# Performance work log

Hardware: AMD Instinct MI355X
Metric: run time of the kernel (lower is better)

The kernel has to match this reference:

```python
import jax, jax.numpy as jnp
import numpy as np

NUM_ROUTES = 1152
NUM_CAPS = 10
CAPS_IN = 8
CAPS_DIM = 16
BATCH = 128
NUM_IT = 3


def _squash(s):
    # s: [..., caps_dim]; scale = |s|^2 / ((1+|s|^2) * |s|)
    sqn = jnp.sum(s * s, axis=-1, keepdims=True)
    return s * (sqn / ((1.0 + sqn) * jnp.sqrt(sqn)))


def setup_inputs() -> dict:
    key = jax.random.key(0)
    k1, k2 = jax.random.split(key)
    x = jax.random.normal(k1, (BATCH, NUM_ROUTES, CAPS_IN), dtype=jnp.float32)
    W = jax.random.normal(k2, (1, NUM_ROUTES, NUM_CAPS, CAPS_DIM, CAPS_IN), dtype=jnp.float32)
    return {"input": x, "W": W}


def reference(input, W):
    # u_hat[b,r,j,d] = W[r,j,d,c] @ x[b,r,c]  (original broadcasts W over batch)
    u_hat = jnp.einsum('rjdc,brc->brjd', W[0], input)
    r, j = u_hat.shape[1], u_hat.shape[2]
    b_ij = jnp.zeros((r, j), dtype=u_hat.dtype)  # shared across batch, as in original
    v = None
    for _ in range(NUM_IT):
        c_ij = jax.nn.softmax(b_ij, axis=1)          # softmax over num_caps (dim=2 orig)
        s = jnp.einsum('rj,brjd->bjd', c_ij, u_hat)  # weighted sum over routes
        v = _squash(s)                                # [bs, num_caps, caps_dim]
        # agreement: <u_hat, v> averaged over batch (original updates every iter)
        b_ij = b_ij + jnp.mean(jnp.einsum('brjd,bjd->brj', u_hat, v), axis=0)
    return v[..., None]  # [bs, num_caps, caps_dim, 1], matches v_j.squeeze(1) shape
```

## Files before the change

### kernel.cpp

```cpp
#include <hip/hip_runtime.h>
#include <math.h>

#define R_ROUTES 1152
#define N_CAPS 10
#define C_IN 8
#define D_DIM 16
#define B_BATCH 128
#define JD 160
#define KK 9216
#define KSPLIT 48
#define RS 24
#define NG 5
#define BH 2

typedef __attribute__((ext_vector_type(8))) short short8;
typedef __attribute__((ext_vector_type(4))) float f32x4;

__device__ inline unsigned short f2bf(float f) {
    unsigned int u = __float_as_uint(f);
    unsigned int r = u + 0x7FFFu + ((u >> 16) & 1u);
    return (unsigned short)(r >> 16);
}
__device__ inline float bf2f(unsigned short h) {
    return __uint_as_float(((unsigned int)h) << 16);
}


__global__ __launch_bounds__(256) void k_prep0(
    const float* __restrict__ x, const float* __restrict__ W,
    unsigned short* __restrict__ xT, f32x4* __restrict__ zbase) {
    __shared__ float tile[32][33];
    int id = blockIdx.x, t = threadIdx.x;
    if (id < 288) {
        int bx = id;
        int tx = t & 31, ty = t >> 5;
        for (int by = 0; by < 4; by++) {
            if (by) __syncthreads();
#pragma unroll
            for (int i = 0; i < 4; i++) {
                int row = ty + i * 8;
                tile[row][tx] = x[(size_t)(by * 32 + row) * KK + bx * 32 + tx];
            }
            __syncthreads();
#pragma unroll
            for (int i = 0; i < 4; i++) {
                int row = ty + i * 8;
                xT[(size_t)(bx * 32 + row) * B_BATCH + by * 32 + tx] = f2bf(tile[tx][row]);
            }
        }
        return;
    }
    if (id < 348) {
        int idx = (id - 288) * 256 + t;
        zbase[idx] = (f32x4){0.f, 0.f, 0.f, 0.f};
        return;
    }
    int wb = id - 348;
    const f32x4* wp = (const f32x4*)W;
    size_t base = (size_t)wb * 3840 + t;
#pragma unroll
    for (int i = 0; i < 15; i++) {
        f32x4 v = wp[base + i * 256];
        asm volatile("" :: "v"(v[0]), "v"(v[1]), "v"(v[2]), "v"(v[3]));
    }
}

template <int FIRST>
__global__ __launch_bounds__(256) void k_iter(
    const float* __restrict__ x, const float* __restrict__ W,
    const float* __restrict__ ctab, float* __restrict__ s) {
    int t = threadIdx.x;
    int ks = blockIdx.x, ng = blockIdx.y, bh = blockIdx.z;
    int r0 = ks * RS, jd0 = ng * 32, b_base = bh * 64;
    int w = t >> 6, l = t & 63, row = l & 15, quad = l >> 4;
    const float* px = x + (size_t)(b_base + w * 16 + row) * KK + ks * 192;
    f32x4 acc0 = {0,0,0,0}, acc1 = {0,0,0,0};
#pragma unroll
    for (int st = 0; st < 6; st++) {
        int rr = r0 + st * 4 + quad;
        float c0 = FIRST ? 0.1f : ctab[rr * N_CAPS + (jd0 >> 4)];
        float c1 = FIRST ? 0.1f : ctab[rr * N_CAPS + (jd0 >> 4) + 1];
        const float4* wp0 = (const float4*)(W + ((size_t)rr * JD + jd0 + row) * C_IN);
        const float4* wp1 = (const float4*)(W + ((size_t)rr * JD + jd0 + 16 + row) * C_IN);
        float4 wa = wp0[0], wb = wp0[1], wc = wp1[0], wd = wp1[1];
        float wv0[8] = {wa.x,wa.y,wa.z,wa.w, wb.x,wb.y,wb.z,wb.w};
        float wv1[8] = {wc.x,wc.y,wc.z,wc.w, wd.x,wd.y,wd.z,wd.w};
        short8 Bh0, Bh1;
#pragma unroll
        for (int i = 0; i < 8; i++) {
            Bh0[i] = (short)f2bf(wv0[i] * c0);
            Bh1[i] = (short)f2bf(wv1[i] * c1);
        }
        float4 x0 = *(const float4*)(px + st * 32 + quad * 8);
        float4 x1 = *(const float4*)(px + st * 32 + quad * 8 + 4);
        float xv[8] = {x0.x,x0.y,x0.z,x0.w, x1.x,x1.y,x1.z,x1.w};
        short8 Ah, Al;
#pragma unroll
        for (int i = 0; i < 8; i++) {
            unsigned short h = f2bf(xv[i]);
            Ah[i] = (short)h;
            Al[i] = (short)f2bf(xv[i] - bf2f(h));
        }
        acc0 = __builtin_amdgcn_mfma_f32_16x16x32_bf16(Ah, Bh0, acc0, 0, 0, 0);
        acc0 = __builtin_amdgcn_mfma_f32_16x16x32_bf16(Al, Bh0, acc0, 0, 0, 0);
        acc1 = __builtin_amdgcn_mfma_f32_16x16x32_bf16(Ah, Bh1, acc1, 0, 0, 0);
        acc1 = __builtin_amdgcn_mfma_f32_16x16x32_bf16(Al, Bh1, acc1, 0, 0, 0);
    }
#pragma unroll
    for (int i = 0; i < 4; i++) {
        int b0 = b_base + w * 16 + quad * 4 + i;
        atomicAdd(&s[(size_t)b0 * JD + jd0 + row],      acc0[i]);
        atomicAdd(&s[(size_t)b0 * JD + jd0 + 16 + row], acc1[i]);
    }
}

template <int ACCUM>
__global__ __launch_bounds__(256) void k_va(
    const unsigned short* __restrict__ xT, const float* __restrict__ s_prev,
    const float* __restrict__ W, float* __restrict__ b_ij,
    float* __restrict__ ctab) {
    __shared__ unsigned short vb[JD][136];
    __shared__ float bnew[4][N_CAPS];
    int t = threadIdx.x;
    int r0 = blockIdx.x * 4, rc0 = blockIdx.x * 32;

#pragma unroll
    for (int q = 0; q < 5; q++) {
        int pi = t * 5 + q;
        int b = pi / N_CAPS, j = pi % N_CAPS;
        const float4* sp4 = (const float4*)(s_prev + (size_t)b * JD + j * D_DIM);
        float4 a0 = sp4[0], a1 = sp4[1], a2 = sp4[2], a3 = sp4[3];
        float sv[D_DIM] = {a0.x,a0.y,a0.z,a0.w, a1.x,a1.y,a1.z,a1.w,
                           a2.x,a2.y,a2.z,a2.w, a3.x,a3.y,a3.z,a3.w};
        float sqn = 0.f;
#pragma unroll
        for (int d = 0; d < D_DIM; d++) sqn = fmaf(sv[d], sv[d], sqn);
        float scale = sqn / ((1.f + sqn) * sqrtf(sqn));
#pragma unroll
        for (int d = 0; d < D_DIM; d++)
            vb[j * D_DIM + d][b] = f2bf(sv[d] * scale);
    }
    __syncthreads();

    int w = t >> 6, l = t & 63, row = l & 15, quad = l >> 4;
    int rhalf = l >> 5, cbase = (quad & 1) * 4;

#pragma unroll
    for (int jt = 0; jt < 5; jt++) {
        int u = jt * 4 + w;
        int mt = u / 10, nt = u % 10;
        const short8* pa = (const short8*)(xT + (size_t)(rc0 + mt * 16 + row) * B_BATCH);
        f32x4 acc = {0, 0, 0, 0};
#pragma unroll
        for (int st = 0; st < 4; st++)
            acc = __builtin_amdgcn_mfma_f32_16x16x32_bf16(
                pa[st * 4 + quad],
                *(const short8*)&vb[nt * 16 + row][st * 32 + quad * 8],
                acc, 0, 0, 0);
        int r = r0 + 2 * mt + rhalf;
        const float* wp = W + ((size_t)r * JD + nt * 16 + row) * C_IN + cbase;
        float4 w4 = *(const float4*)wp;
        float part = acc[0]*w4.x + acc[1]*w4.y + acc[2]*w4.z + acc[3]*w4.w;
#pragma unroll
        for (int off = 1; off < 32; off <<= 1) part += __shfl_xor(part, off, 32);
        if ((l & 31) == 0) bnew[2 * mt + rhalf][nt] = part * (1.f / (float)B_BATCH);
    }
    __syncthreads();

    if (t < 4) {
        float bj[N_CAPS], m = -1e30f;
#pragma unroll
        for (int j = 0; j < N_CAPS; j++) {
            float base = ACCUM ? b_ij[(r0 + t) * N_CAPS + j] : 0.f;
            bj[j] = base + bnew[t][j];
            m = fmaxf(m, bj[j]);
        }
        if (!ACCUM) {
#pragma unroll
            for (int j = 0; j < N_CAPS; j++) b_ij[(r0 + t) * N_CAPS + j] = bj[j];
        }
        float sum = 0.f;
#pragma unroll
        for (int j = 0; j < N_CAPS; j++) { bj[j] = expf(bj[j] - m); sum += bj[j]; }
        float inv = 1.f / sum;
#pragma unroll
        for (int j = 0; j < N_CAPS; j++) ctab[(r0 + t) * N_CAPS + j] = bj[j] * inv;
    }
}

__global__ __launch_bounds__(320) void k_rs_final(
    const float* __restrict__ s, float* __restrict__ out) {
    int t = threadIdx.x;
    int bloc = t / JD, jd = t % JD;
    int b = blockIdx.x * 2 + bloc;
    float acc = s[(size_t)b * JD + jd];
    float sq = acc * acc;
#pragma unroll
    for (int off = 1; off < 16; off <<= 1) sq += __shfl_xor(sq, off, 16);
    float scale = sq / ((1.f + sq) * sqrtf(sq));
    out[(size_t)b * JD + jd] = acc * scale;
}

extern "C" void kernel_launch(void* const* d_in, const int* in_sizes, int n_in,
                              void* d_out, int out_size, void* d_ws, size_t ws_size,
                              hipStream_t stream) {
    const float* x = (const float*)d_in[0];
    const float* W = (const float*)d_in[1];
    float* out = (float*)d_out;
    char* ws = (char*)d_ws;

    float*          s0   = (float*)(ws + 0);
    float*          s1   = (float*)(ws + 81920);
    float*          s2   = (float*)(ws + 163840);
    float*          b_ij = (float*)(ws + 245760);
    float*          ctab = (float*)(ws + 291840);
    unsigned short* xT   = (unsigned short*)(ws + 337920);

    k_prep0<<<444, 256, 0, stream>>>(x, W, xT, (f32x4*)ws);

    k_iter<1><<<dim3(KSPLIT, NG, BH), 256, 0, stream>>>(x, W, nullptr, s0);

    k_va<0><<<288, 256, 0, stream>>>(xT, s0, W, b_ij, ctab);

    k_iter<0><<<dim3(KSPLIT, NG, BH), 256, 0, stream>>>(x, W, ctab, s1);

    k_va<1><<<288, 256, 0, stream>>>(xT, s1, W, b_ij, ctab);

    k_iter<0><<<dim3(KSPLIT, NG, BH), 256, 0, stream>>>(x, W, ctab, s2);

    k_rs_final<<<64, 320, 0, stream>>>(s2, out);
}
```

Baseline: 115.2 us.

## Raise grid parallelism across prep, iteration and agreement kernels; drop W prefetch

The route split in k_iter doubles (96 blocks along K, each covering 12 routes), which doubles the atomicAdd traffic into s. k_va now handles 2 routes per block across 576 blocks and loads its A fragments once before the capsule loop. k_prep0 gives each 32x32 transpose tile its own block and no longer runs the W L2-prewarm blocks. The aim is more concurrent blocks to fill the GPU's compute units; the costs are extra atomics, the repeated vb squash setup in every k_va block, and losing the warmed W cache.

After: 126.2 us. 9.6% more time.

```diff
diff --git a/kernel.cpp b/kernel.cpp
--- a/kernel.cpp
+++ b/kernel.cpp
@@ -8,8 +8,8 @@
 #define B_BATCH 128
 #define JD 160
 #define KK 9216
-#define KSPLIT 48
-#define RS 24
+#define KSPLIT 96
+#define RS 12
 #define NG 5
 #define BH 2
 
@@ -27,42 +27,28 @@
 
 
 __global__ __launch_bounds__(256) void k_prep0(
-    const float* __restrict__ x, const float* __restrict__ W,
-    unsigned short* __restrict__ xT, f32x4* __restrict__ zbase) {
+    const float* __restrict__ x, unsigned short* __restrict__ xT,
+    f32x4* __restrict__ zbase) {
     __shared__ float tile[32][33];
     int id = blockIdx.x, t = threadIdx.x;
-    if (id < 288) {
-        int bx = id;
+    if (id < 1152) {
+        int bx = id % 288, by = id / 288;
         int tx = t & 31, ty = t >> 5;
-        for (int by = 0; by < 4; by++) {
-            if (by) __syncthreads();
-#pragma unroll
-            for (int i = 0; i < 4; i++) {
-                int row = ty + i * 8;
-                tile[row][tx] = x[(size_t)(by * 32 + row) * KK + bx * 32 + tx];
-            }
-            __syncthreads();
-#pragma unroll
-            for (int i = 0; i < 4; i++) {
-                int row = ty + i * 8;
-                xT[(size_t)(bx * 32 + row) * B_BATCH + by * 32 + tx] = f2bf(tile[tx][row]);
-            }
+#pragma unroll
+        for (int i = 0; i < 4; i++) {
+            int row = ty + i * 8;
+            tile[row][tx] = x[(size_t)(by * 32 + row) * KK + bx * 32 + tx];
+        }
+        __syncthreads();
+#pragma unroll
+        for (int i = 0; i < 4; i++) {
+            int row = ty + i * 8;
+            xT[(size_t)(bx * 32 + row) * B_BATCH + by * 32 + tx] = f2bf(tile[tx][row]);
         }
         return;
     }
-    if (id < 348) {
-        int idx = (id - 288) * 256 + t;
-        zbase[idx] = (f32x4){0.f, 0.f, 0.f, 0.f};
-        return;
-    }
-    int wb = id - 348;
-    const f32x4* wp = (const f32x4*)W;
-    size_t base = (size_t)wb * 3840 + t;
-#pragma unroll
-    for (int i = 0; i < 15; i++) {
-        f32x4 v = wp[base + i * 256];
-        asm volatile("" :: "v"(v[0]), "v"(v[1]), "v"(v[2]), "v"(v[3]));
-    }
+    int idx = (id - 1152) * 256 + t;
+    zbase[idx] = (f32x4){0.f, 0.f, 0.f, 0.f};
 }
 
 template <int FIRST>
@@ -73,10 +59,10 @@
     int ks = blockIdx.x, ng = blockIdx.y, bh = blockIdx.z;
     int r0 = ks * RS, jd0 = ng * 32, b_base = bh * 64;
     int w = t >> 6, l = t & 63, row = l & 15, quad = l >> 4;
-    const float* px = x + (size_t)(b_base + w * 16 + row) * KK + ks * 192;
+    const float* px = x + (size_t)(b_base + w * 16 + row) * KK + ks * 96;
     f32x4 acc0 = {0,0,0,0}, acc1 = {0,0,0,0};
 #pragma unroll
-    for (int st = 0; st < 6; st++) {
+    for (int st = 0; st < 3; st++) {
         int rr = r0 + st * 4 + quad;
         float c0 = FIRST ? 0.1f : ctab[rr * N_CAPS + (jd0 >> 4)];
         float c1 = FIRST ? 0.1f : ctab[rr * N_CAPS + (jd0 >> 4) + 1];
@@ -120,9 +106,9 @@
     const float* __restrict__ W, float* __restrict__ b_ij,
     float* __restrict__ ctab) {
     __shared__ unsigned short vb[JD][136];
-    __shared__ float bnew[4][N_CAPS];
+    __shared__ float bnew[2][N_CAPS];
     int t = threadIdx.x;
-    int r0 = blockIdx.x * 4, rc0 = blockIdx.x * 32;
+    int r0 = blockIdx.x * 2, rc0 = blockIdx.x * 16;
 
 #pragma unroll
     for (int q = 0; q < 5; q++) {
@@ -145,29 +131,29 @@
     int w = t >> 6, l = t & 63, row = l & 15, quad = l >> 4;
     int rhalf = l >> 5, cbase = (quad & 1) * 4;
 
-#pragma unroll
-    for (int jt = 0; jt < 5; jt++) {
-        int u = jt * 4 + w;
-        int mt = u / 10, nt = u % 10;
-        const short8* pa = (const short8*)(xT + (size_t)(rc0 + mt * 16 + row) * B_BATCH);
+    const short8* pa = (const short8*)(xT + (size_t)(rc0 + row) * B_BATCH);
+    short8 af0 = pa[quad], af1 = pa[4 + quad], af2 = pa[8 + quad], af3 = pa[12 + quad];
+    for (int nt = w; nt < N_CAPS; nt += 4) {
         f32x4 acc = {0, 0, 0, 0};
-#pragma unroll
-        for (int st = 0; st < 4; st++)
-            acc = __builtin_amdgcn_mfma_f32_16x16x32_bf16(
-                pa[st * 4 + quad],
-                *(const short8*)&vb[nt * 16 + row][st * 32 + quad * 8],
-                acc, 0, 0, 0);
-        int r = r0 + 2 * mt + rhalf;
+        acc = __builtin_amdgcn_mfma_f32_16x16x32_bf16(
+            af0, *(const short8*)&vb[nt * 16 + row][quad * 8], acc, 0, 0, 0);
+        acc = __builtin_amdgcn_mfma_f32_16x16x32_bf16(
+            af1, *(const short8*)&vb[nt * 16 + row][32 + quad * 8], acc, 0, 0, 0);
+        acc = __builtin_amdgcn_mfma_f32_16x16x32_bf16(
+            af2, *(const short8*)&vb[nt * 16 + row][64 + quad * 8], acc, 0, 0, 0);
+        acc = __builtin_amdgcn_mfma_f32_16x16x32_bf16(
+            af3, *(const short8*)&vb[nt * 16 + row][96 + quad * 8], acc, 0, 0, 0);
+        int r = r0 + rhalf;
         const float* wp = W + ((size_t)r * JD + nt * 16 + row) * C_IN + cbase;
         float4 w4 = *(const float4*)wp;
         float part = acc[0]*w4.x + acc[1]*w4.y + acc[2]*w4.z + acc[3]*w4.w;
 #pragma unroll
         for (int off = 1; off < 32; off <<= 1) part += __shfl_xor(part, off, 32);
-        if ((l & 31) == 0) bnew[2 * mt + rhalf][nt] = part * (1.f / (float)B_BATCH);
+        if ((l & 31) == 0) bnew[rhalf][nt] = part * (1.f / (float)B_BATCH);
     }
     __syncthreads();
 
-    if (t < 4) {
+    if (t < 2) {
         float bj[N_CAPS], m = -1e30f;
 #pragma unroll
         for (int j = 0; j < N_CAPS; j++) {
@@ -216,15 +202,15 @@
     float*          ctab = (float*)(ws + 291840);
     unsigned short* xT   = (unsigned short*)(ws + 337920);
 
-    k_prep0<<<444, 256, 0, stream>>>(x, W, xT, (f32x4*)ws);
+    k_prep0<<<1212, 256, 0, stream>>>(x, xT, (f32x4*)ws);
 
     k_iter<1><<<dim3(KSPLIT, NG, BH), 256, 0, stream>>>(x, W, nullptr, s0);
 
-    k_va<0><<<288, 256, 0, stream>>>(xT, s0, W, b_ij, ctab);
+    k_va<0><<<576, 256, 0, stream>>>(xT, s0, W, b_ij, ctab);
 
     k_iter<0><<<dim3(KSPLIT, NG, BH), 256, 0, stream>>>(x, W, ctab, s1);
 
-    k_va<1><<<288, 256, 0, stream>>>(xT, s1, W, b_ij, ctab);
+    k_va<1><<<576, 256, 0, stream>>>(xT, s1, W, b_ij, ctab);
 
     k_iter<0><<<dim3(KSPLIT, NG, BH), 256, 0, stream>>>(x, W, ctab, s2);
 
```
